# Kernel tuning notes

Hardware: AMD Instinct MI355X
Metric: run time of the kernel (lower is better)

The kernel has to match this reference:

```python
import jax, jax.numpy as jnp
import numpy as np

D_MODEL = 96
D_STATE = 16
D_CONV = 3
EXPAND = 2
D_INNER = D_MODEL * EXPAND          # 192
DT_RANK = max(1, D_MODEL // 16)     # 6
N_DIRS = 4
LN_EPS = 1e-5


def setup_inputs() -> dict:
    key = jax.random.key(0)
    ks = jax.random.split(key, 10)
    B, H, W = 2, 64, 64
    x = jax.random.normal(ks[0], (B, D_MODEL, H, W), dtype=jnp.float32)
    in_proj_w = jax.random.normal(ks[1], (2 * D_INNER, D_MODEL), dtype=jnp.float32) * 0.02
    conv_w = jax.random.normal(ks[2], (D_INNER, 1, D_CONV, D_CONV), dtype=jnp.float32) * 0.1
    conv_b = jnp.zeros((D_INNER,), dtype=jnp.float32)
    proj_dim = DT_RANK + 2 * D_STATE
    x_proj_weight = jax.random.normal(ks[3], (N_DIRS, D_INNER, proj_dim), dtype=jnp.float32) * 0.02
    dt_proj_weight = jax.random.normal(ks[4], (N_DIRS, D_INNER, DT_RANK), dtype=jnp.float32) * 0.02
    dt_proj_bias = jax.random.uniform(ks[5], (N_DIRS, D_INNER), dtype=jnp.float32) * 0.1
    A_log = jnp.log(jnp.broadcast_to(jnp.arange(1, D_STATE + 1, dtype=jnp.float32), (D_INNER, D_STATE)))
    D_skip = jnp.ones((D_INNER,), dtype=jnp.float32)
    ln_gamma = jnp.ones((D_INNER,), dtype=jnp.float32)
    ln_beta = jnp.zeros((D_INNER,), dtype=jnp.float32)
    out_proj_w = jax.random.normal(ks[6], (D_MODEL, D_INNER), dtype=jnp.float32) * 0.02
    return {
        "x": x, "in_proj_w": in_proj_w, "conv_w": conv_w, "conv_b": conv_b,
        "x_proj_weight": x_proj_weight, "dt_proj_weight": dt_proj_weight,
        "dt_proj_bias": dt_proj_bias, "A_log": A_log, "D_skip": D_skip,
        "ln_gamma": ln_gamma, "ln_beta": ln_beta, "out_proj_w": out_proj_w,
    }


def _ss2d_forward(x, in_proj_w, conv_w, conv_b, x_proj_weight, dt_proj_weight,
                  dt_proj_bias, A_log, D_skip, ln_gamma, ln_beta, out_proj_w):
    B, D, H, W = x.shape
    E, N, R = D_INNER, D_STATE, DT_RANK
    L = H * W
    # in_proj
    x_flat = x.reshape(B, D, L).transpose(0, 2, 1)              # b l d
    xz = x_flat @ in_proj_w.T                                    # b l 2e
    xb, z = xz[..., :E], xz[..., E:]
    # depthwise conv + SiLU
    xb = xb.transpose(0, 2, 1).reshape(B, E, H, W)
    xb = jax.lax.conv_general_dilated(
        xb, conv_w, window_strides=(1, 1), padding="SAME",
        feature_group_count=E, dimension_numbers=("NCHW", "OIHW", "NCHW"))
    xb = xb + conv_b[None, :, None, None]
    xb = jax.nn.silu(xb)
    # 4-directional cross-scan sequences
    x_rm = xb.reshape(B, E, L)
    x_cm = xb.transpose(0, 1, 3, 2).reshape(B, E, L)
    xs = jnp.stack([x_rm, x_rm[..., ::-1], x_cm, x_cm[..., ::-1]], axis=0)  # k b e l
    # per-direction projections
    x_for = xs.transpose(0, 1, 3, 2)                             # k b l e
    x_dbl = jnp.einsum("kble,ker->kblr", x_for, x_proj_weight)
    dt_low, Bs, Cs = x_dbl[..., :R], x_dbl[..., R:R + N], x_dbl[..., R + N:]
    dts = jnp.einsum("kblr,ker->kble", dt_low, dt_proj_weight) + dt_proj_bias[:, None, None, :]
    dt = jax.nn.softplus(dts)                                    # k b l e
    A = -jnp.exp(A_log)                                          # e n
    # batched selective scan over (k*b)
    KB = N_DIRS * B
    u = xs.reshape(KB, E, L)
    dt_ = dt.transpose(0, 1, 3, 2).reshape(KB, E, L)
    B_t = Bs.reshape(KB, L, N)
    C_t = Cs.reshape(KB, L, N)
    deltaA = jnp.exp(dt_[..., None] * A[None, :, None, :])       # kb e l n
    deltaBx = (dt_ * u)[..., None] * B_t[:, None, :, :]          # kb e l n

    def comb(c1, c2):
        a1, b1 = c1
        a2, b2 = c2
        return (a2 * a1, a2 * b1 + b2)

    _, h = jax.lax.associative_scan(comb, (deltaA, deltaBx), axis=2)  # kb e l n
    y = jnp.einsum("beln,bln->bel", h, C_t) + u * D_skip[None, :, None]
    ys = y.reshape(N_DIRS, B, E, L)
    y0, y1, y2, y3 = ys[0], ys[1][..., ::-1], ys[2], ys[3][..., ::-1]
    y_row = (y0 + y1).reshape(B, E, H, W)
    y_col = (y2 + y3).reshape(B, E, W, H).transpose(0, 1, 3, 2)
    yo = (y_row + y_col).reshape(B, E, L).transpose(0, 2, 1)     # b l e
    # LayerNorm over e
    mu = jnp.mean(yo, axis=-1, keepdims=True)
    var = jnp.mean((yo - mu) ** 2, axis=-1, keepdims=True)
    yo = (yo - mu) * jax.lax.rsqrt(var + LN_EPS) * ln_gamma + ln_beta
    yo = yo * jax.nn.silu(z)
    out = yo @ out_proj_w.T                                      # b l d
    return out.transpose(0, 2, 1).reshape(B, D, H, W)


def reference(x, in_proj_w, conv_w, conv_b, x_proj_weight, dt_proj_weight,
              dt_proj_bias, A_log, D_skip, ln_gamma, ln_beta, out_proj_w):
    return _ss2d_forward(x, in_proj_w, conv_w, conv_b, x_proj_weight,
                         dt_proj_weight, dt_proj_bias, A_log, D_skip,
                         ln_gamma, ln_beta, out_proj_w)
```

## Files before the change

### kernel.cpp

```cpp
#include <hip/hip_runtime.h>

#define LL 4096
#define HH 64
#define WWD 64
#define DM 96
#define EE 192
#define NN 16
#define RR 6
#define KBB 8
#define BB 2
#define CH 128
#define CLEN 32
#define SID (KBB * EE * NN)

__global__ __launch_bounds__(256) void k_inproj(const float* __restrict__ x,
                                                const float* __restrict__ W,
                                                float* __restrict__ xbuf,
                                                float* __restrict__ zbuf) {
    __shared__ float As[96][64];
    __shared__ float Ws[96][64];
    int bm = blockIdx.x;
    int bn = blockIdx.y;
    int l0 = bm * 64;
    int b  = l0 >> 12;
    int lb = l0 & (LL - 1);
    int j0 = bn * 64;
    int t  = threadIdx.x;

    for (int i = t; i < 96 * 64; i += 256) {
        int d = i >> 6, ml = i & 63;
        As[d][ml] = x[((size_t)b * 96 + d) * LL + lb + ml];
    }
    for (int i = t; i < 96 * 64; i += 256) {
        int jn = i / 96, d = i - jn * 96;
        Ws[d][jn] = W[(size_t)(j0 + jn) * 96 + d];
    }
    __syncthreads();

    int tx = t & 15, ty = t >> 4;
    float acc[4][4] = {};
    for (int d = 0; d < 96; d++) {
        float a[4], bbv[4];
        for (int i = 0; i < 4; i++) a[i] = As[d][ty * 4 + i];
        for (int j = 0; j < 4; j++) bbv[j] = Ws[d][tx * 4 + j];
        for (int i = 0; i < 4; i++)
            for (int j = 0; j < 4; j++) acc[i][j] = fmaf(a[i], bbv[j], acc[i][j]);
    }
    for (int i = 0; i < 4; i++) {
        int l = lb + ty * 4 + i;
        for (int j = 0; j < 4; j++) {
            int jj = j0 + tx * 4 + j;
            if (jj < EE)
                xbuf[((size_t)b * EE + jj) * LL + l] = acc[i][j];
            else
                zbuf[((size_t)b * LL + l) * EE + (jj - EE)] = acc[i][j];
        }
    }
}

__global__ __launch_bounds__(256) void k_conv(const float* __restrict__ xbuf,
                                              const float* __restrict__ cw,
                                              const float* __restrict__ cb,
                                              float* __restrict__ xconv,
                                              float* __restrict__ xconv_t) {
    __shared__ float T[32][33];
    int l0 = blockIdx.x * 32;
    int e0 = blockIdx.y * 32;
    int b  = blockIdx.z;
    int t  = threadIdx.x;
    int tp = t & 31, teo = t >> 5;

    int pos = l0 + tp;
    int h = pos >> 6, w = pos & 63;
    #pragma unroll
    for (int j = 0; j < 4; j++) {
        int ee = j * 8 + teo;
        int e = e0 + ee;
        const float* src = xbuf + ((size_t)b * EE + e) * LL;
        const float* wgt = cw + e * 9;
        float acc = cb[e];
        #pragma unroll
        for (int dh = -1; dh <= 1; dh++) {
            int hh = h + dh;
            if (hh < 0 || hh >= HH) continue;
            #pragma unroll
            for (int dw = -1; dw <= 1; dw++) {
                int w2 = w + dw;
                if (w2 < 0 || w2 >= WWD) continue;
                acc = fmaf(src[hh * WWD + w2], wgt[(dh + 1) * 3 + (dw + 1)], acc);
            }
        }
        float v = acc / (1.f + __expf(-acc));
        xconv[((size_t)b * EE + e) * LL + pos] = v;
        T[ee][tp] = v;
    }
    __syncthreads();
    for (int i = t; i < 32 * 32; i += 256) {
        int p = i >> 5, ee = i & 31;
        xconv_t[((size_t)b * LL + l0 + p) * EE + e0 + ee] = T[ee][p];
    }
}

__device__ __forceinline__ int seq_of_spatial(int k, int idx) {
    if (k == 0) return idx;
    if (k == 1) return LL - 1 - idx;
    int p = ((idx & 63) << 6) | (idx >> 6);
    if (k == 2) return p;
    return LL - 1 - p;
}

__device__ __forceinline__ int spatial_of_seq(int k, int l) {
    int lp = (k & 1) ? (LL - 1 - l) : l;
    return (k >= 2) ? (((lp & 63) << 6) | (lp >> 6)) : lp;
}

__global__ __launch_bounds__(256) void k_proj(const float* __restrict__ xconv,
                                              const float* __restrict__ xpw,
                                              const float* __restrict__ dtw,
                                              const float* __restrict__ dtb,
                                              float* __restrict__ dtbuf,
                                              float* __restrict__ Bbuf,
                                              float* __restrict__ Cbuf) {
    __shared__ float Ws[32][161];
    __shared__ float PR[4][32][8];
    __shared__ float BC[4][32][33];
    int l0 = blockIdx.x * 32;
    int b  = blockIdx.y;
    int t  = threadIdx.x;
    int pg = t >> 5;
    int oc = t & 31;

    float acc[4][5] = {};

    for (int ep = 0; ep < 6; ep++) {
        int e0 = ep * 32;
        __syncthreads();
        for (int i = t; i < 4 * 32 * 38; i += 256) {
            int k = i / 1216;
            int rem = i - k * 1216;
            int ee = rem / 38, r = rem - ee * 38;
            Ws[ee][k * 38 + r] = xpw[((size_t)k * EE + e0 + ee) * 38 + r];
        }
        for (int i = t; i < 32 * 9; i += 256) {
            int ee = i / 9;
            Ws[ee][152 + i % 9] = 0.f;
        }
        __syncthreads();
        #pragma unroll 8
        for (int ee = 0; ee < 32; ee++) {
            int e = e0 + ee;
            float4 xv = *(const float4*)&xconv[((size_t)b * EE + e) * LL + l0 + 4 * pg];
            float wv[5];
            #pragma unroll
            for (int j = 0; j < 5; j++) wv[j] = Ws[ee][oc + 32 * j];
            #pragma unroll
            for (int j = 0; j < 5; j++) {
                acc[0][j] = fmaf(xv.x, wv[j], acc[0][j]);
                acc[1][j] = fmaf(xv.y, wv[j], acc[1][j]);
                acc[2][j] = fmaf(xv.z, wv[j], acc[2][j]);
                acc[3][j] = fmaf(xv.w, wv[j], acc[3][j]);
            }
        }
    }

    #pragma unroll
    for (int j = 0; j < 5; j++) {
        int col = oc + 32 * j;
        if (col < 152) {
            int k = (col >= 114) ? 3 : (col >= 76) ? 2 : (col >= 38) ? 1 : 0;
            int r = col - k * 38;
            #pragma unroll
            for (int ii = 0; ii < 4; ii++) {
                int pos = 4 * pg + ii;
                if (r < 6) PR[k][pos][r] = acc[ii][j];
                else       BC[k][pos][r - 6] = acc[ii][j];
            }
        }
    }
    __syncthreads();

    for (int i = t; i < 4 * 32 * 32; i += 256) {
        int kk = i >> 10;
        int pos = (i >> 5) & 31;
        int c = i & 31;
        int j = seq_of_spatial(kk, l0 + pos);
        float v = BC[kk][pos][c];
        int kb = kk * 2 + b;
        if (c < 16) Bbuf[((size_t)kb * LL + j) * NN + c] = v;
        else        Cbuf[((size_t)kb * LL + j) * NN + (c - 16)] = v;
    }

    for (int i = t; i < 4 * 32 * EE; i += 256) {
        int kp = i / EE;
        int e = i - kp * EE;
        int kk = kp >> 5, pos = kp & 31;
        float s = dtb[kk * EE + e];
        const float* wr = dtw + ((size_t)kk * EE + e) * RR;
        #pragma unroll
        for (int r = 0; r < RR; r++) s = fmaf(PR[kk][pos][r], wr[r], s);
        float sp = (s > 20.f) ? s : log1pf(__expf(s));
        int j = seq_of_spatial(kk, l0 + pos);
        int kb = kk * 2 + b;
        dtbuf[((size_t)kb * LL + j) * EE + e] = sp;
    }
}

__global__ __launch_bounds__(192) void k_scan1(const float* __restrict__ xconv_t,
                                               const float* __restrict__ dtbuf,
                                               const float* __restrict__ Bbuf,
                                               const float* __restrict__ A_log,
                                               float* __restrict__ Ap,
                                               float* __restrict__ He) {
    __shared__ __align__(16) float sB[CLEN][NN];
    int c  = blockIdx.x;
    int kb = blockIdx.y;
    int k = kb >> 1, b = kb & 1;
    int e = threadIdx.x;
    int l0 = c * CLEN;

    for (int i = e; i < CLEN * NN; i += 192)
        ((float*)sB)[i] = Bbuf[((size_t)kb * LL + l0) * NN + i];

    float An[NN], h[NN], pa[NN];
    #pragma unroll
    for (int q = 0; q < 4; q++) {
        float4 al = *(const float4*)&A_log[e * NN + q * 4];
        An[q*4+0] = -__expf(al.x); An[q*4+1] = -__expf(al.y);
        An[q*4+2] = -__expf(al.z); An[q*4+3] = -__expf(al.w);
    }
    #pragma unroll
    for (int n = 0; n < NN; n++) { h[n] = 0.f; pa[n] = 1.f; }
    __syncthreads();

    const float* dtp = dtbuf + ((size_t)kb * LL + l0) * EE + e;
    const float* ub  = xconv_t + (size_t)b * LL * EE + e;

    #pragma unroll 2
    for (int i = 0; i < CLEN; i++) {
        int l = l0 + i;
        int idx = spatial_of_seq(k, l);
        float dtv = dtp[(size_t)i * EE];
        float u   = ub[(size_t)idx * EE];
        float Bv[NN];
        #pragma unroll
        for (int q = 0; q < 4; q++)
            *(float4*)&Bv[q*4] = ((const float4*)&sB[i][0])[q];
        float dtu = dtv * u;
        #pragma unroll
        for (int n = 0; n < NN; n++) {
            float a = __expf(dtv * An[n]);
            h[n] = fmaf(a, h[n], dtu * Bv[n]);
            pa[n] *= a;
        }
    }
    size_t sid = (size_t)c * SID + kb * (EE * NN) + e * NN;
    #pragma unroll
    for (int q = 0; q < 4; q++) {
        *(float4*)&Ap[sid + q*4] = make_float4(pa[q*4], pa[q*4+1], pa[q*4+2], pa[q*4+3]);
        *(float4*)&He[sid + q*4] = make_float4(h[q*4], h[q*4+1], h[q*4+2], h[q*4+3]);
    }
}

__global__ __launch_bounds__(256) void k_carry(float* __restrict__ ApHi,
                                               const float* __restrict__ He) {
    int sid = blockIdx.x * 256 + threadIdx.x;
    float h = 0.f;
    #pragma unroll 8
    for (int c = 0; c < CH; c++) {
        size_t ix = (size_t)c * SID + sid;
        float a  = ApHi[ix];
        float he = He[ix];
        ApHi[ix] = h;
        h = fmaf(a, h, he);
    }
}

__global__ __launch_bounds__(192) void k_scan2(const float* __restrict__ xconv_t,
                                               const float* __restrict__ dtbuf,
                                               const float* __restrict__ Bbuf,
                                               const float* __restrict__ Cbuf,
                                               const float* __restrict__ A_log,
                                               const float* __restrict__ Dskip,
                                               const float* __restrict__ Hi,
                                               float* __restrict__ yo) {
    __shared__ __align__(16) float sB[CLEN][NN];
    __shared__ __align__(16) float sC[CLEN][NN];
    int c  = blockIdx.x;
    int kb = blockIdx.y;
    int k = kb >> 1, b = kb & 1;
    int e = threadIdx.x;
    int l0 = c * CLEN;

    for (int i = e; i < CLEN * NN; i += 192) {
        ((float*)sB)[i] = Bbuf[((size_t)kb * LL + l0) * NN + i];
        ((float*)sC)[i] = Cbuf[((size_t)kb * LL + l0) * NN + i];
    }

    float An[NN], h[NN];
    #pragma unroll
    for (int q = 0; q < 4; q++) {
        float4 al = *(const float4*)&A_log[e * NN + q * 4];
        An[q*4+0] = -__expf(al.x); An[q*4+1] = -__expf(al.y);
        An[q*4+2] = -__expf(al.z); An[q*4+3] = -__expf(al.w);
    }
    size_t sid = (size_t)c * SID + kb * (EE * NN) + e * NN;
    #pragma unroll
    for (int q = 0; q < 4; q++) {
        float4 hv = *(const float4*)&Hi[sid + q*4];
        h[q*4+0] = hv.x; h[q*4+1] = hv.y; h[q*4+2] = hv.z; h[q*4+3] = hv.w;
    }
    float Dv = Dskip[e];
    __syncthreads();

    const float* dtp = dtbuf + ((size_t)kb * LL + l0) * EE + e;
    const float* ub  = xconv_t + (size_t)b * LL * EE + e;
    float* yob       = yo + (size_t)b * LL * EE + e;

    #pragma unroll 2
    for (int i = 0; i < CLEN; i++) {
        int l = l0 + i;
        int idx = spatial_of_seq(k, l);
        float dtv = dtp[(size_t)i * EE];
        float u   = ub[(size_t)idx * EE];
        float Bv[NN], Cv[NN];
        #pragma unroll
        for (int q = 0; q < 4; q++) {
            *(float4*)&Bv[q*4] = ((const float4*)&sB[i][0])[q];
            *(float4*)&Cv[q*4] = ((const float4*)&sC[i][0])[q];
        }
        float dtu = dtv * u;
        float y = u * Dv;
        #pragma unroll
        for (int n = 0; n < NN; n++) {
            float a = __expf(dtv * An[n]);
            h[n] = fmaf(a, h[n], dtu * Bv[n]);
            y = fmaf(h[n], Cv[n], y);
        }
        atomicAdd(&yob[(size_t)idx * EE], y);
    }
}

__global__ __launch_bounds__(256) void k_out(const float* __restrict__ yo,
                                             const float* __restrict__ zb,
                                             const float* __restrict__ gamma,
                                             const float* __restrict__ beta,
                                             const float* __restrict__ W2,
                                             float* __restrict__ out) {
    __shared__ float sbuf[32][193];
    int b  = blockIdx.x >> 7;
    int l0 = (blockIdx.x & 127) * 32;
    int t  = threadIdx.x;
    int wv = t >> 6, lane = t & 63;

    for (int li = 0; li < 32; li += 4) {
        int l = l0 + li + wv;
        const float* yrow = yo + ((size_t)b * LL + l) * EE;
        const float* zrow = zb + ((size_t)b * LL + l) * EE;
        float v[3], zv[3];
        float s = 0.f;
        #pragma unroll
        for (int j = 0; j < 3; j++) {
            v[j] = yrow[lane + 64 * j];
            zv[j] = zrow[lane + 64 * j];
            s += v[j];
        }
        for (int m = 1; m < 64; m <<= 1) s += __shfl_xor(s, m);
        float mu = s * (1.f / EE);
        float q = 0.f;
        #pragma unroll
        for (int j = 0; j < 3; j++) { float d = v[j] - mu; q = fmaf(d, d, q); }
        for (int m = 1; m < 64; m <<= 1) q += __shfl_xor(q, m);
        float rs = rsqrtf(q * (1.f / EE) + 1e-5f);
        #pragma unroll
        for (int j = 0; j < 3; j++) {
            int e = lane + 64 * j;
            float yn = (v[j] - mu) * rs * gamma[e] + beta[e];
            float zz = zv[j];
            float sil = zz / (1.f + __expf(-zz));
            sbuf[li + wv][e] = yn * sil;
        }
    }
    __syncthreads();
    for (int o = t; o < DM * 32; o += 256) {
        int d = o >> 5, c = o & 31;
        const float* wr = W2 + (size_t)d * EE;
        float acc = 0.f;
        for (int e = 0; e < EE; e++) acc = fmaf(sbuf[c][e], wr[e], acc);
        out[((size_t)b * DM + d) * LL + l0 + c] = acc;
    }
}

extern "C" void kernel_launch(void* const* d_in, const int* in_sizes, int n_in,
                              void* d_out, int out_size, void* d_ws, size_t ws_size,
                              hipStream_t stream) {
    const float* x      = (const float*)d_in[0];
    const float* in_w   = (const float*)d_in[1];
    const float* conv_w = (const float*)d_in[2];
    const float* conv_b = (const float*)d_in[3];
    const float* xpw    = (const float*)d_in[4];
    const float* dtw    = (const float*)d_in[5];
    const float* dtbias = (const float*)d_in[6];
    const float* A_log  = (const float*)d_in[7];
    const float* Dsk    = (const float*)d_in[8];
    const float* gamma  = (const float*)d_in[9];
    const float* beta   = (const float*)d_in[10];
    const float* W2     = (const float*)d_in[11];
    float* out = (float*)d_out;

    float* ws      = (float*)d_ws;
    float* xbuf    = ws;
    float* zbuf    = xbuf    + (size_t)BB * EE * LL;
    float* xconv   = zbuf    + (size_t)BB * LL * EE;
    float* xconv_t = xconv   + (size_t)BB * EE * LL;
    float* dtbuf   = xconv_t + (size_t)BB * LL * EE;
    float* Bbuf    = dtbuf   + (size_t)KBB * LL * EE;
    float* Cbuf    = Bbuf    + (size_t)KBB * LL * NN;
    float* yo      = Cbuf    + (size_t)KBB * LL * NN;
    float* ApHi    = yo      + (size_t)BB * LL * EE;
    float* He      = ApHi    + (size_t)CH * SID;

    hipMemsetAsync(yo, 0, (size_t)BB * LL * EE * sizeof(float), stream);

    k_inproj<<<dim3(128, 6), 256, 0, stream>>>(x, in_w, xbuf, zbuf);
    k_conv<<<dim3(128, 6, 2), 256, 0, stream>>>(xbuf, conv_w, conv_b, xconv, xconv_t);
    k_proj<<<dim3(128, 2), 256, 0, stream>>>(xconv, xpw, dtw, dtbias, dtbuf, Bbuf, Cbuf);
    k_scan1<<<dim3(CH, KBB), 192, 0, stream>>>(xconv_t, dtbuf, Bbuf, A_log, ApHi, He);
    k_carry<<<SID / 256, 256, 0, stream>>>(ApHi, He);
    k_scan2<<<dim3(CH, KBB), 192, 0, stream>>>(xconv_t, dtbuf, Bbuf, Cbuf, A_log, Dsk, ApHi, yo);
    k_out<<<BB * (LL / 32), 256, 0, stream>>>(yo, zbuf, gamma, beta, W2, out);
}
```

Baseline: 316.5 us.

## Replace scan atomics with per-direction outputs, split k_proj by direction, alias workspace

k_scan2 now writes each direction's output to its own sequence-ordered buffer with plain stores instead of atomicAdd scattered into a shared spatial buffer. k_out gathers and sums the four directions itself, which also removes the memset. k_proj gains a grid dimension over directions, so each block computes one direction's 38 columns straight from global weights without the shared-memory weight staging. Workspace regions are aliased (xbuf/xconv/He reuse the ys region) to shrink the footprint. The trade-off is more global reads in k_out and redundant xconv reads across the four k_proj direction blocks.

```diff
diff --git a/kernel.cpp b/kernel.cpp
--- a/kernel.cpp
+++ b/kernel.cpp
@@ -121,86 +121,65 @@
                                               float* __restrict__ dtbuf,
                                               float* __restrict__ Bbuf,
                                               float* __restrict__ Cbuf) {
-    __shared__ float Ws[32][161];
-    __shared__ float PR[4][32][8];
-    __shared__ float BC[4][32][33];
+    __shared__ float PR[32][8];
+    __shared__ float BC[32][33];
     int l0 = blockIdx.x * 32;
     int b  = blockIdx.y;
+    int k  = blockIdx.z;
     int t  = threadIdx.x;
     int pg = t >> 5;
     int oc = t & 31;
 
-    float acc[4][5] = {};
-
-    for (int ep = 0; ep < 6; ep++) {
-        int e0 = ep * 32;
-        __syncthreads();
-        for (int i = t; i < 4 * 32 * 38; i += 256) {
-            int k = i / 1216;
-            int rem = i - k * 1216;
-            int ee = rem / 38, r = rem - ee * 38;
-            Ws[ee][k * 38 + r] = xpw[((size_t)k * EE + e0 + ee) * 38 + r];
-        }
-        for (int i = t; i < 32 * 9; i += 256) {
-            int ee = i / 9;
-            Ws[ee][152 + i % 9] = 0.f;
-        }
-        __syncthreads();
-        #pragma unroll 8
-        for (int ee = 0; ee < 32; ee++) {
-            int e = e0 + ee;
-            float4 xv = *(const float4*)&xconv[((size_t)b * EE + e) * LL + l0 + 4 * pg];
-            float wv[5];
-            #pragma unroll
-            for (int j = 0; j < 5; j++) wv[j] = Ws[ee][oc + 32 * j];
-            #pragma unroll
-            for (int j = 0; j < 5; j++) {
-                acc[0][j] = fmaf(xv.x, wv[j], acc[0][j]);
-                acc[1][j] = fmaf(xv.y, wv[j], acc[1][j]);
-                acc[2][j] = fmaf(xv.z, wv[j], acc[2][j]);
-                acc[3][j] = fmaf(xv.w, wv[j], acc[3][j]);
-            }
-        }
-    }
-
-    #pragma unroll
-    for (int j = 0; j < 5; j++) {
-        int col = oc + 32 * j;
-        if (col < 152) {
-            int k = (col >= 114) ? 3 : (col >= 76) ? 2 : (col >= 38) ? 1 : 0;
-            int r = col - k * 38;
-            #pragma unroll
-            for (int ii = 0; ii < 4; ii++) {
-                int pos = 4 * pg + ii;
-                if (r < 6) PR[k][pos][r] = acc[ii][j];
-                else       BC[k][pos][r - 6] = acc[ii][j];
-            }
-        }
-    }
-    __syncthreads();
-
-    for (int i = t; i < 4 * 32 * 32; i += 256) {
-        int kk = i >> 10;
-        int pos = (i >> 5) & 31;
-        int c = i & 31;
-        int j = seq_of_spatial(kk, l0 + pos);
-        float v = BC[kk][pos][c];
-        int kb = kk * 2 + b;
+    const float* wbase = xpw + (size_t)k * EE * 38;
+    const float* xbase = xconv + (size_t)b * EE * LL + l0 + 4 * pg;
+
+    float acc0[4] = {}, acc1[4] = {};
+    #pragma unroll 4
+    for (int e = 0; e < EE; e++) {
+        float4 xv = *(const float4*)&xbase[(size_t)e * LL];
+        const float* wrow = wbase + e * 38;
+        float w0 = wrow[oc];
+        float w1 = (oc < 6) ? wrow[oc + 32] : 0.f;
+        acc0[0] = fmaf(xv.x, w0, acc0[0]);
+        acc0[1] = fmaf(xv.y, w0, acc0[1]);
+        acc0[2] = fmaf(xv.z, w0, acc0[2]);
+        acc0[3] = fmaf(xv.w, w0, acc0[3]);
+        acc1[0] = fmaf(xv.x, w1, acc1[0]);
+        acc1[1] = fmaf(xv.y, w1, acc1[1]);
+        acc1[2] = fmaf(xv.z, w1, acc1[2]);
+        acc1[3] = fmaf(xv.w, w1, acc1[3]);
+    }
+
+    #pragma unroll
+    for (int ii = 0; ii < 4; ii++) {
+        int p = 4 * pg + ii;
+        if (oc < 6) {
+            PR[p][oc] = acc0[ii];
+            BC[p][oc + 26] = acc1[ii];
+        } else {
+            BC[p][oc - 6] = acc0[ii];
+        }
+    }
+    __syncthreads();
+
+    int kb = k * 2 + b;
+    for (int i = t; i < 32 * 32; i += 256) {
+        int pos = i >> 5, c = i & 31;
+        int j = seq_of_spatial(k, l0 + pos);
+        float v = BC[pos][c];
         if (c < 16) Bbuf[((size_t)kb * LL + j) * NN + c] = v;
         else        Cbuf[((size_t)kb * LL + j) * NN + (c - 16)] = v;
     }
 
-    for (int i = t; i < 4 * 32 * EE; i += 256) {
-        int kp = i / EE;
-        int e = i - kp * EE;
-        int kk = kp >> 5, pos = kp & 31;
-        float s = dtb[kk * EE + e];
-        const float* wr = dtw + ((size_t)kk * EE + e) * RR;
-        #pragma unroll
-        for (int r = 0; r < RR; r++) s = fmaf(PR[kk][pos][r], wr[r], s);
+    for (int i = t; i < 32 * EE; i += 256) {
+        int pos = i / EE;
+        int e = i - pos * EE;
+        float s = dtb[k * EE + e];
+        const float* wr = dtw + ((size_t)k * EE + e) * RR;
+        #pragma unroll
+        for (int r = 0; r < RR; r++) s = fmaf(PR[pos][r], wr[r], s);
         float sp = (s > 20.f) ? s : log1pf(__expf(s));
-        int j = seq_of_spatial(kk, l0 + pos);
-        int kb = kk * 2 + b;
+        int j = seq_of_spatial(k, l0 + pos);
         dtbuf[((size_t)kb * LL + j) * EE + e] = sp;
     }
 }
@@ -282,7 +261,7 @@
                                                const float* __restrict__ A_log,
                                                const float* __restrict__ Dskip,
                                                const float* __restrict__ Hi,
-                                               float* __restrict__ yo) {
+                                               float* __restrict__ ys) {
     __shared__ __align__(16) float sB[CLEN][NN];
     __shared__ __align__(16) float sC[CLEN][NN];
     int c  = blockIdx.x;
@@ -314,7 +293,7 @@
 
     const float* dtp = dtbuf + ((size_t)kb * LL + l0) * EE + e;
     const float* ub  = xconv_t + (size_t)b * LL * EE + e;
-    float* yob       = yo + (size_t)b * LL * EE + e;
+    float* ysb       = ys + ((size_t)kb * LL + l0) * EE + e;
 
     #pragma unroll 2
     for (int i = 0; i < CLEN; i++) {
@@ -336,11 +315,11 @@
             h[n] = fmaf(a, h[n], dtu * Bv[n]);
             y = fmaf(h[n], Cv[n], y);
         }
-        atomicAdd(&yob[(size_t)idx * EE], y);
-    }
-}
-
-__global__ __launch_bounds__(256) void k_out(const float* __restrict__ yo,
+        ysb[(size_t)i * EE] = y;
+    }
+}
+
+__global__ __launch_bounds__(256) void k_out(const float* __restrict__ ys,
                                              const float* __restrict__ zb,
                                              const float* __restrict__ gamma,
                                              const float* __restrict__ beta,
@@ -354,14 +333,19 @@
 
     for (int li = 0; li < 32; li += 4) {
         int l = l0 + li + wv;
-        const float* yrow = yo + ((size_t)b * LL + l) * EE;
+        int p = ((l & 63) << 6) | (l >> 6);
+        const float* r0 = ys + ((size_t)(0 + b) * LL + l) * EE;
+        const float* r1 = ys + ((size_t)(2 + b) * LL + (LL - 1 - l)) * EE;
+        const float* r2 = ys + ((size_t)(4 + b) * LL + p) * EE;
+        const float* r3 = ys + ((size_t)(6 + b) * LL + (LL - 1 - p)) * EE;
         const float* zrow = zb + ((size_t)b * LL + l) * EE;
         float v[3], zv[3];
         float s = 0.f;
         #pragma unroll
         for (int j = 0; j < 3; j++) {
-            v[j] = yrow[lane + 64 * j];
-            zv[j] = zrow[lane + 64 * j];
+            int e = lane + 64 * j;
+            v[j] = r0[e] + r1[e] + r2[e] + r3[e];
+            zv[j] = zrow[e];
             s += v[j];
         }
         for (int m = 1; m < 64; m <<= 1) s += __shfl_xor(s, m);
@@ -408,24 +392,23 @@
     float* out = (float*)d_out;
 
     float* ws      = (float*)d_ws;
-    float* xbuf    = ws;
-    float* zbuf    = xbuf    + (size_t)BB * EE * LL;
-    float* xconv   = zbuf    + (size_t)BB * LL * EE;
-    float* xconv_t = xconv   + (size_t)BB * EE * LL;
+    float* zbuf    = ws;
+    float* xconv_t = zbuf    + (size_t)BB * LL * EE;
     float* dtbuf   = xconv_t + (size_t)BB * LL * EE;
     float* Bbuf    = dtbuf   + (size_t)KBB * LL * EE;
     float* Cbuf    = Bbuf    + (size_t)KBB * LL * NN;
-    float* yo      = Cbuf    + (size_t)KBB * LL * NN;
-    float* ApHi    = yo      + (size_t)BB * LL * EE;
-    float* He      = ApHi    + (size_t)CH * SID;
-
-    hipMemsetAsync(yo, 0, (size_t)BB * LL * EE * sizeof(float), stream);
+    float* ApHi    = Cbuf    + (size_t)KBB * LL * NN;
+    float* R       = ApHi    + (size_t)CH * SID;
+    float* ys      = R;
+    float* xbuf    = R;
+    float* xconv   = R + (size_t)BB * EE * LL;
+    float* He      = R + 2 * (size_t)BB * EE * LL;
 
     k_inproj<<<dim3(128, 6), 256, 0, stream>>>(x, in_w, xbuf, zbuf);
     k_conv<<<dim3(128, 6, 2), 256, 0, stream>>>(xbuf, conv_w, conv_b, xconv, xconv_t);
-    k_proj<<<dim3(128, 2), 256, 0, stream>>>(xconv, xpw, dtw, dtbias, dtbuf, Bbuf, Cbuf);
+    k_proj<<<dim3(128, 2, 4), 256, 0, stream>>>(xconv, xpw, dtw, dtbias, dtbuf, Bbuf, Cbuf);
     k_scan1<<<dim3(CH, KBB), 192, 0, stream>>>(xconv_t, dtbuf, Bbuf, A_log, ApHi, He);
     k_carry<<<SID / 256, 256, 0, stream>>>(ApHi, He);
-    k_scan2<<<dim3(CH, KBB), 192, 0, stream>>>(xconv_t, dtbuf, Bbuf, Cbuf, A_log, Dsk, ApHi, yo);
-    k_out<<<BB * (LL / 32), 256, 0, stream>>>(yo, zbuf, gamma, beta, W2, out);
-}
+    k_scan2<<<dim3(CH, KBB), 192, 0, stream>>>(xconv_t, dtbuf, Bbuf, Cbuf, A_log, Dsk, ApHi, ys);
+    k_out<<<BB * (LL / 32), 256, 0, stream>>>(ys, zbuf, gamma, beta, W2, out);
+}
```

Measured after the change: 289.5 us. 8.5% less time.
